# Optimization experiments

Hardware: AMD Instinct MI355X
Metric: run time of the kernel (lower is better)

## Reference

```python
import jax, jax.numpy as jnp
import numpy as np

B, N, U = 4, 4096, 512


def setup_inputs() -> dict:
    key = jax.random.key(0)
    ks = jax.random.split(key, 5)
    s = 1.0 / np.sqrt(U)
    return {
        "x": jax.random.normal(ks[0], (B, N, U), dtype=jnp.float32),
        "Wq": jax.random.normal(ks[1], (U, U), dtype=jnp.float32) * s,
        "bq": jnp.zeros((U,), dtype=jnp.float32),
        "Wk": jax.random.normal(ks[2], (U, U), dtype=jnp.float32) * s,
        "bk": jnp.zeros((U,), dtype=jnp.float32),
        "Wv": jax.random.normal(ks[3], (U, U), dtype=jnp.float32) * s,
        "bv": jnp.zeros((U,), dtype=jnp.float32),
        "Wp": jax.random.normal(ks[4], (U, U), dtype=jnp.float32) * s,
        "bp": jnp.zeros((U,), dtype=jnp.float32),
    }


def reference(x, Wq, bq, Wk, bk, Wv, bv, Wp, bp):
    # x: [B, N, U] single-head self-attention with residual
    scale = jnp.asarray(x.shape[-1], jnp.float32) ** -0.5
    q = x @ Wq + bq
    k = x @ Wk + bk
    v = x @ Wv + bv
    scores = jnp.einsum("bnd,bmd->bnm", q, k) * scale  # [B, N, N]
    attn = jax.nn.softmax(scores, axis=-1)
    ctx = jnp.einsum("bnm,bmd->bnd", attn, v)
    return x + (ctx @ Wp + bp)
```

## Files before the change

kernel.cpp:

```cpp
#include <hip/hip_runtime.h>
#include <hip/hip_bf16.h>
#include <math.h>

#define NB 4
#define NN 4096
#define UU 512

using short8  = __attribute__((ext_vector_type(8))) short;
using bf16x8  = __attribute__((ext_vector_type(8))) __bf16;
using floatx4 = __attribute__((ext_vector_type(4))) float;

__device__ __forceinline__ floatx4 mfma16(short8 a, short8 b, floatx4 c) {
    return __builtin_amdgcn_mfma_f32_16x16x32_bf16(
        __builtin_bit_cast(bf16x8, a), __builtin_bit_cast(bf16x8, b), c, 0, 0, 0);
}

__device__ __forceinline__ unsigned short f2bf(float f) {
    union { float f; unsigned u; } v; v.f = f;
    return (unsigned short)((v.u + 0x7fffu + ((v.u >> 16) & 1u)) >> 16);
}
__device__ __forceinline__ float bf2f(unsigned short s) {
    union { unsigned u; float f; } v; v.u = ((unsigned)s) << 16; return v.f;
}

#define GLL16(gp, lp) __builtin_amdgcn_global_load_lds( \
    (const __attribute__((address_space(1))) void*)(gp), \
    (__attribute__((address_space(3))) void*)(lp), 16, 0, 0)

__global__ void __launch_bounds__(256) k_cvt_x(const float* __restrict__ x,
                                               unsigned short* __restrict__ xb) {
    int i = (blockIdx.x * 256 + threadIdx.x) * 4;
    float4 v = *(const float4*)(x + i);
    ushort4 o;
    o.x = f2bf(v.x); o.y = f2bf(v.y); o.z = f2bf(v.z); o.w = f2bf(v.w);
    *(ushort4*)(xb + i) = o;
}

__global__ void __launch_bounds__(256) k_cvt_w(const float* __restrict__ W,
                                               unsigned short* __restrict__ WT) {
    int idx = blockIdx.x * 256 + threadIdx.x;
    int n = idx >> 9, k = idx & 511;
    WT[idx] = f2bf(W[k * 512 + n]);
}

__global__ void __launch_bounds__(256, 2) k_proj(
    const unsigned short* __restrict__ Xb,
    const unsigned short* __restrict__ WqT, const unsigned short* __restrict__ WkT,
    const unsigned short* __restrict__ WvT,
    const float* __restrict__ bq, const float* __restrict__ bk, const float* __restrict__ bv,
    unsigned short* __restrict__ Q, unsigned short* __restrict__ K8,
    unsigned short* __restrict__ V8)
{
    __shared__ __align__(16) unsigned short As[128 * 32];
    __shared__ __align__(16) unsigned short Bs[128 * 32];
    const int z = blockIdx.z;
    const unsigned short* WT = (z == 0) ? WqT : (z == 1) ? WkT : WvT;
    const float* bias = (z == 0) ? bq : (z == 1) ? bk : bv;
    const int t = threadIdx.x, wave = t >> 6, lane = t & 63;
    const int quad = lane >> 4, l16 = lane & 15;
    const int m0 = blockIdx.x * 128, n0 = blockIdx.y * 128;
    const int wm = wave >> 1, wn = wave & 1;

    const int srow = wave * 32 + (lane >> 2);
    const int scol = (lane & 3) * 8;
    const unsigned short* gA = Xb + (size_t)(m0 + srow) * UU + scol;
    const unsigned short* gB = WT + (size_t)(n0 + srow) * UU + scol;
    unsigned short* lA = As + wave * 1024;
    unsigned short* lB = Bs + wave * 1024;

    floatx4 acc[4][4] = {};

    for (int k0 = 0; k0 < UU; k0 += 32) {
        GLL16(gA + k0, lA);
        GLL16(gA + k0 + 16 * UU, lA + 512);
        GLL16(gB + k0, lB);
        GLL16(gB + k0 + 16 * UU, lB + 512);
        __syncthreads();
        short8 a[4], b[4];
        #pragma unroll
        for (int i = 0; i < 4; i++)
            a[i] = *(const short8*)(As + (wm * 64 + i * 16 + l16) * 32 + quad * 8);
        #pragma unroll
        for (int j = 0; j < 4; j++)
            b[j] = *(const short8*)(Bs + (wn * 64 + j * 16 + l16) * 32 + quad * 8);
        #pragma unroll
        for (int i = 0; i < 4; i++)
            #pragma unroll
            for (int j = 0; j < 4; j++)
                acc[i][j] = mfma16(a[i], b[j], acc[i][j]);
        __syncthreads();
    }

    #pragma unroll
    for (int j = 0; j < 4; j++) {
        const int n = n0 + wn * 64 + j * 16 + l16;
        const float bv_ = bias[n];
        #pragma unroll
        for (int i = 0; i < 4; i++) {
            const int mb = m0 + wm * 64 + i * 16 + quad * 4;
            const int bb = mb >> 12, tok = mb & (NN - 1);
            if (z == 0) {
                #pragma unroll
                for (int r = 0; r < 4; r++)
                    Q[(size_t)(mb + r) * UU + n] = f2bf(acc[i][j][r] + bv_);
            } else if (z == 1) {
                const size_t base = (size_t)bb * NN * UU + (size_t)(n >> 3) * (NN * 8)
                                  + (size_t)tok * 8 + (n & 7);
                #pragma unroll
                for (int r = 0; r < 4; r++)
                    K8[base + (size_t)r * 8] = f2bf(acc[i][j][r] + bv_);
            } else {
                ushort4 o;
                o.x = f2bf(acc[i][j][0] + bv_);
                o.y = f2bf(acc[i][j][1] + bv_);
                o.z = f2bf(acc[i][j][2] + bv_);
                o.w = f2bf(acc[i][j][3] + bv_);
                *(ushort4*)(V8 + (size_t)bb * NN * UU + (size_t)(tok >> 3) * (UU * 8)
                            + (size_t)n * 8 + (tok & 7)) = o;
            }
        }
    }
}

__global__ void __launch_bounds__(512, 1) k_flash(
    const unsigned short* __restrict__ Q,
    const unsigned short* __restrict__ K8,
    const unsigned short* __restrict__ V8,
    unsigned short* __restrict__ ctx)
{
    __shared__ __align__(16) unsigned short Ks[64 * 64 * 8];
    __shared__ __align__(16) unsigned short Vs[8 * 512 * 8];
    __shared__ __align__(16) float S_lds[64 * 68];
    __shared__ __align__(16) unsigned short P_lds[64 * 72];
    __shared__ float m_lds[64], l_lds[64], a_lds[64];

    const int b = blockIdx.y;
    const int q0 = blockIdx.x * 64;
    const int t = threadIdx.x;
    const int wave = t >> 6, lane = t & 63, quad = lane >> 4, l16 = lane & 15;
    const int qt = wave >> 1;
    const int kh = wave & 1;
    const int dh = wave & 1;

    if (t < 64) { m_lds[t] = -INFINITY; l_lds[t] = 0.f; }

    const unsigned short* qp = Q + (size_t)(b * NN + q0 + qt * 16 + l16) * UU + quad * 8;
    short8 qf[16];
    #pragma unroll
    for (int kk = 0; kk < 16; kk++) qf[kk] = *(const short8*)(qp + kk * 32);

    const unsigned short* K8b = K8 + (size_t)b * NN * UU;
    const unsigned short* V8b = V8 + (size_t)b * NN * UU;

    #pragma unroll
    for (int j = 0; j < 8; j++) {
        const int dc = wave * 8 + j;
        GLL16(K8b + (size_t)dc * (NN * 8) + lane * 8, Ks + dc * 512 + lane * 8);
    }

    floatx4 o[16] = {};
    const float sscale = 0.04419417382415922f * 1.4426950408889634f;

    __syncthreads();

    for (int kt = 0; kt < NN; kt += 64) {
        #pragma unroll
        for (int j = 0; j < 8; j++) {
            const int c = wave * 8 + j;
            GLL16(V8b + (size_t)kt * 512 + (size_t)c * 512 + lane * 8, Vs + c * 512 + lane * 8);
        }

        floatx4 s0 = {}, s1 = {};
        #pragma unroll
        for (int kk = 0; kk < 16; kk++) {
            const unsigned short* kb = Ks + (kk * 4 + quad) * 512 + (kh * 32 + l16) * 8;
            short8 b0 = *(const short8*)(kb);
            short8 b1 = *(const short8*)(kb + 128);
            s0 = mfma16(qf[kk], b0, s0);
            s1 = mfma16(qf[kk], b1, s1);
        }
        #pragma unroll
        for (int i = 0; i < 4; i++) {
            S_lds[(qt * 16 + quad * 4 + i) * 68 + kh * 32 + l16]      = s0[i] * sscale;
            S_lds[(qt * 16 + quad * 4 + i) * 68 + kh * 32 + 16 + l16] = s1[i] * sscale;
        }
        __syncthreads();

        {
            const int row = t >> 3, c8 = (t & 7) * 8;
            const float4* sp = (const float4*)(S_lds + row * 68 + c8);
            float4 va = sp[0], vb = sp[1];
            float mx = fmaxf(fmaxf(fmaxf(va.x, va.y), fmaxf(va.z, va.w)),
                             fmaxf(fmaxf(vb.x, vb.y), fmaxf(vb.z, vb.w)));
            mx = fmaxf(mx, __shfl_xor(mx, 1, 8));
            mx = fmaxf(mx, __shfl_xor(mx, 2, 8));
            mx = fmaxf(mx, __shfl_xor(mx, 4, 8));
            const float m_old = m_lds[row];
            const float m_new = fmaxf(m_old, mx);
            float p[8] = { exp2f(va.x - m_new), exp2f(va.y - m_new),
                           exp2f(va.z - m_new), exp2f(va.w - m_new),
                           exp2f(vb.x - m_new), exp2f(vb.y - m_new),
                           exp2f(vb.z - m_new), exp2f(vb.w - m_new) };
            short8 pv; float sum = 0.f;
            #pragma unroll
            for (int j = 0; j < 8; j++) {
                unsigned short us = f2bf(p[j]);
                pv[j] = (short)us;
                sum += bf2f(us);
            }
            *(short8*)(P_lds + row * 72 + c8) = pv;
            sum += __shfl_xor(sum, 1, 8);
            sum += __shfl_xor(sum, 2, 8);
            sum += __shfl_xor(sum, 4, 8);
            if ((t & 7) == 0) {
                const float alpha = exp2f(m_old - m_new);
                a_lds[row] = alpha;
                m_lds[row] = m_new;
                l_lds[row] = l_lds[row] * alpha + sum;
            }
        }
        __syncthreads();

        if (kt + 64 < NN) {
            #pragma unroll
            for (int j = 0; j < 8; j++) {
                const int dc = wave * 8 + j;
                GLL16(K8b + (size_t)dc * (NN * 8) + (size_t)(kt + 64 + lane) * 8,
                      Ks + dc * 512 + lane * 8);
            }
        }

        float al[4];
        #pragma unroll
        for (int i = 0; i < 4; i++) al[i] = a_lds[qt * 16 + quad * 4 + i];
        #pragma unroll
        for (int dt = 0; dt < 16; dt++)
            #pragma unroll
            for (int i = 0; i < 4; i++) o[dt][i] *= al[i];
        const short8 a0 = *(const short8*)(P_lds + (qt * 16 + l16) * 72 + quad * 8);
        const short8 a1 = *(const short8*)(P_lds + (qt * 16 + l16) * 72 + 32 + quad * 8);
        #pragma unroll
        for (int dt = 0; dt < 16; dt++) {
            const int d = dh * 256 + dt * 16 + l16;
            short8 b0 = *(const short8*)(Vs + quad * 4096 + d * 8);
            short8 b1 = *(const short8*)(Vs + (4 + quad) * 4096 + d * 8);
            o[dt] = mfma16(a0, b0, o[dt]);
            o[dt] = mfma16(a1, b1, o[dt]);
        }
        __syncthreads();
    }

    float linv[4];
    #pragma unroll
    for (int i = 0; i < 4; i++) linv[i] = 1.f / l_lds[qt * 16 + quad * 4 + i];
    #pragma unroll
    for (int dt = 0; dt < 16; dt++) {
        const int d = dh * 256 + dt * 16 + l16;
        #pragma unroll
        for (int i = 0; i < 4; i++)
            ctx[(size_t)(b * NN + q0 + qt * 16 + quad * 4 + i) * UU + d] = f2bf(o[dt][i] * linv[i]);
    }
}

__global__ void __launch_bounds__(256, 2) k_out(
    const unsigned short* __restrict__ Cx,
    const unsigned short* __restrict__ WpT,
    const float* __restrict__ bp,
    const float* __restrict__ x,
    float* __restrict__ out)
{
    __shared__ __align__(16) unsigned short As[128 * 32];
    __shared__ __align__(16) unsigned short Bs[128 * 32];
    const int t = threadIdx.x, wave = t >> 6, lane = t & 63;
    const int quad = lane >> 4, l16 = lane & 15;
    const int m0 = blockIdx.x * 128, n0 = blockIdx.y * 128;
    const int wm = wave >> 1, wn = wave & 1;
    const int srow = wave * 32 + (lane >> 2);
    const int scol = (lane & 3) * 8;
    const unsigned short* gA = Cx + (size_t)(m0 + srow) * UU + scol;
    const unsigned short* gB = WpT + (size_t)(n0 + srow) * UU + scol;
    unsigned short* lA = As + wave * 1024;
    unsigned short* lB = Bs + wave * 1024;

    floatx4 acc[4][4] = {};

    for (int k0 = 0; k0 < UU; k0 += 32) {
        GLL16(gA + k0, lA);
        GLL16(gA + k0 + 16 * UU, lA + 512);
        GLL16(gB + k0, lB);
        GLL16(gB + k0 + 16 * UU, lB + 512);
        __syncthreads();
        short8 a[4], b[4];
        #pragma unroll
        for (int i = 0; i < 4; i++)
            a[i] = *(const short8*)(As + (wm * 64 + i * 16 + l16) * 32 + quad * 8);
        #pragma unroll
        for (int j = 0; j < 4; j++)
            b[j] = *(const short8*)(Bs + (wn * 64 + j * 16 + l16) * 32 + quad * 8);
        #pragma unroll
        for (int i = 0; i < 4; i++)
            #pragma unroll
            for (int j = 0; j < 4; j++)
                acc[i][j] = mfma16(a[i], b[j], acc[i][j]);
        __syncthreads();
    }

    #pragma unroll
    for (int j = 0; j < 4; j++) {
        const int n = n0 + wn * 64 + j * 16 + l16;
        const float bv_ = bp[n];
        #pragma unroll
        for (int i = 0; i < 4; i++) {
            const int mb = m0 + wm * 64 + i * 16 + quad * 4;
            #pragma unroll
            for (int r = 0; r < 4; r++) {
                const size_t idx = (size_t)(mb + r) * UU + n;
                out[idx] = acc[i][j][r] + bv_ + x[idx];
            }
        }
    }
}

extern "C" void kernel_launch(void* const* d_in, const int* in_sizes, int n_in,
                              void* d_out, int out_size, void* d_ws, size_t ws_size,
                              hipStream_t stream)
{
    const float* x  = (const float*)d_in[0];
    const float* Wq = (const float*)d_in[1];
    const float* bq = (const float*)d_in[2];
    const float* Wk = (const float*)d_in[3];
    const float* bk = (const float*)d_in[4];
    const float* Wv = (const float*)d_in[5];
    const float* bv = (const float*)d_in[6];
    const float* Wp = (const float*)d_in[7];
    const float* bp = (const float*)d_in[8];
    float* out = (float*)d_out;

    char* ws = (char*)d_ws;
    unsigned short* Xb  = (unsigned short*)(ws);
    unsigned short* WqT = (unsigned short*)(ws + 16777216);
    unsigned short* WkT = (unsigned short*)(ws + 17301504);
    unsigned short* WvT = (unsigned short*)(ws + 17825792);
    unsigned short* WpT = (unsigned short*)(ws + 18350080);
    unsigned short* Qm  = (unsigned short*)(ws + 18874368);
    unsigned short* K8m = (unsigned short*)(ws + 35651584);
    unsigned short* V8m = (unsigned short*)(ws + 52428800);
    unsigned short* Cx  = (unsigned short*)(ws + 69206016);

    hipLaunchKernelGGL(k_cvt_x, dim3(8192), dim3(256), 0, stream, x, Xb);
    hipLaunchKernelGGL(k_cvt_w, dim3(1024), dim3(256), 0, stream, Wq, WqT);
    hipLaunchKernelGGL(k_cvt_w, dim3(1024), dim3(256), 0, stream, Wk, WkT);
    hipLaunchKernelGGL(k_cvt_w, dim3(1024), dim3(256), 0, stream, Wv, WvT);
    hipLaunchKernelGGL(k_cvt_w, dim3(1024), dim3(256), 0, stream, Wp, WpT);
    hipLaunchKernelGGL(k_proj, dim3(128, 4, 3), dim3(256), 0, stream,
                       Xb, WqT, WkT, WvT, bq, bk, bv, Qm, K8m, V8m);
    hipLaunchKernelGGL(k_flash, dim3(64, 4), dim3(512), 0, stream, Qm, K8m, V8m, Cx);
    hipLaunchKernelGGL(k_out, dim3(128, 4), dim3(256), 0, stream, Cx, WpT, bp, x, out);
}
```

Before: 374.6 us.

## Restructure flash kernel waves to split head dim and keys, merge weight conversions

Each wave in the attention kernel now computes two 16-row query tiles over half the head dimension, with QK partial scores combined through LDS atomic adds. Each wave also handles one key half for the PV product, and the two key-half partials are summed through LDS at the end. This is meant to reuse each K and V fragment across two query tiles and so cut LDS reads per MFMA. The cost is atomic adds to shared memory, an extra zeroing pass over the score buffer, and a larger shared-memory footprint (~155KB), which makes the raised launch bound of 2 blocks per CU unlikely to be met. The four weight-conversion launches are also fused into a single launch.

```diff
diff --git a/kernel.cpp b/kernel.cpp
--- a/kernel.cpp
+++ b/kernel.cpp
@@ -36,11 +36,15 @@
     *(ushort4*)(xb + i) = o;
 }
 
-__global__ void __launch_bounds__(256) k_cvt_w(const float* __restrict__ W,
-                                               unsigned short* __restrict__ WT) {
+__global__ void __launch_bounds__(256) k_cvt_w4(
+    const float* __restrict__ Wq, const float* __restrict__ Wk,
+    const float* __restrict__ Wv, const float* __restrict__ Wp,
+    unsigned short* __restrict__ WTbase) {
+    const int z = blockIdx.y;
+    const float* W = (z == 0) ? Wq : (z == 1) ? Wk : (z == 2) ? Wv : Wp;
     int idx = blockIdx.x * 256 + threadIdx.x;
     int n = idx >> 9, k = idx & 511;
-    WT[idx] = f2bf(W[k * 512 + n]);
+    WTbase[(size_t)z * 262144 + idx] = f2bf(W[k * 512 + n]);
 }
 
 __global__ void __launch_bounds__(256, 2) k_proj(
@@ -122,32 +126,42 @@
     }
 }
 
-__global__ void __launch_bounds__(512, 1) k_flash(
+__global__ void __launch_bounds__(512, 2) k_flash(
     const unsigned short* __restrict__ Q,
     const unsigned short* __restrict__ K8,
     const unsigned short* __restrict__ V8,
     unsigned short* __restrict__ ctx)
 {
-    __shared__ __align__(16) unsigned short Ks[64 * 64 * 8];
-    __shared__ __align__(16) unsigned short Vs[8 * 512 * 8];
-    __shared__ __align__(16) float S_lds[64 * 68];
-    __shared__ __align__(16) unsigned short P_lds[64 * 72];
-    __shared__ float m_lds[64], l_lds[64], a_lds[64];
+    __shared__ __align__(16) char smem[158464];
+    unsigned short* Ks = (unsigned short*)smem;
+    unsigned short* Vs = (unsigned short*)(smem + 65536);
+    float*          S_f = (float*)(smem + 131072);
+    unsigned short* P_l = (unsigned short*)(smem + 148480);
+    float*          m_l = (float*)(smem + 157696);
+    float*          l_l = m_l + 64;
+    float*          a_l = m_l + 128;
 
     const int b = blockIdx.y;
     const int q0 = blockIdx.x * 64;
     const int t = threadIdx.x;
     const int wave = t >> 6, lane = t & 63, quad = lane >> 4, l16 = lane & 15;
-    const int qt = wave >> 1;
+    const int qg = wave >> 2;
+    const int half = (wave >> 1) & 1;
     const int kh = wave & 1;
-    const int dh = wave & 1;
-
-    if (t < 64) { m_lds[t] = -INFINITY; l_lds[t] = 0.f; }
-
-    const unsigned short* qp = Q + (size_t)(b * NN + q0 + qt * 16 + l16) * UU + quad * 8;
+
+    if (t < 64) { m_l[t] = -INFINITY; l_l[t] = 0.f; }
+    { const int row = t >> 3, c = (t & 7) * 8;
+      *(float4*)(S_f + row * 68 + c) = float4{0,0,0,0};
+      *(float4*)(S_f + row * 68 + c + 4) = float4{0,0,0,0}; }
+
+    const unsigned short* qp = Q + (size_t)(b * NN + q0 + qg * 32 + l16) * UU
+                             + half * 256 + quad * 8;
     short8 qf[16];
     #pragma unroll
-    for (int kk = 0; kk < 16; kk++) qf[kk] = *(const short8*)(qp + kk * 32);
+    for (int qt = 0; qt < 2; qt++)
+        #pragma unroll
+        for (int kk = 0; kk < 8; kk++)
+            qf[qt * 8 + kk] = *(const short8*)(qp + qt * 16 * UU + kk * 32);
 
     const unsigned short* K8b = K8 + (size_t)b * NN * UU;
     const unsigned short* V8b = V8 + (size_t)b * NN * UU;
@@ -158,7 +172,7 @@
         GLL16(K8b + (size_t)dc * (NN * 8) + lane * 8, Ks + dc * 512 + lane * 8);
     }
 
-    floatx4 o[16] = {};
+    floatx4 o[2][16] = {};
     const float sscale = 0.04419417382415922f * 1.4426950408889634f;
 
     __syncthreads();
@@ -170,32 +184,40 @@
             GLL16(V8b + (size_t)kt * 512 + (size_t)c * 512 + lane * 8, Vs + c * 512 + lane * 8);
         }
 
-        floatx4 s0 = {}, s1 = {};
-        #pragma unroll
-        for (int kk = 0; kk < 16; kk++) {
-            const unsigned short* kb = Ks + (kk * 4 + quad) * 512 + (kh * 32 + l16) * 8;
-            short8 b0 = *(const short8*)(kb);
-            short8 b1 = *(const short8*)(kb + 128);
-            s0 = mfma16(qf[kk], b0, s0);
-            s1 = mfma16(qf[kk], b1, s1);
-        }
-        #pragma unroll
-        for (int i = 0; i < 4; i++) {
-            S_lds[(qt * 16 + quad * 4 + i) * 68 + kh * 32 + l16]      = s0[i] * sscale;
-            S_lds[(qt * 16 + quad * 4 + i) * 68 + kh * 32 + 16 + l16] = s1[i] * sscale;
-        }
+        floatx4 sacc[2][2] = {};
+        #pragma unroll
+        for (int kk = 0; kk < 8; kk++) {
+            #pragma unroll
+            for (int k2 = 0; k2 < 2; k2++) {
+                const int dc = half * 32 + kk * 4 + quad;
+                const int key = kh * 32 + k2 * 16 + l16;
+                short8 bfrag = *(const short8*)(Ks + dc * 512 + key * 8);
+                sacc[0][k2] = mfma16(qf[kk],     bfrag, sacc[0][k2]);
+                sacc[1][k2] = mfma16(qf[8 + kk], bfrag, sacc[1][k2]);
+            }
+        }
+        #pragma unroll
+        for (int qt = 0; qt < 2; qt++)
+            #pragma unroll
+            for (int k2 = 0; k2 < 2; k2++) {
+                const int row = qg * 32 + qt * 16 + quad * 4;
+                const int col = kh * 32 + k2 * 16 + l16;
+                #pragma unroll
+                for (int i = 0; i < 4; i++)
+                    atomicAdd(&S_f[(row + i) * 68 + col], sacc[qt][k2][i] * sscale);
+            }
         __syncthreads();
 
         {
             const int row = t >> 3, c8 = (t & 7) * 8;
-            const float4* sp = (const float4*)(S_lds + row * 68 + c8);
+            const float4* sp = (const float4*)(S_f + row * 68 + c8);
             float4 va = sp[0], vb = sp[1];
             float mx = fmaxf(fmaxf(fmaxf(va.x, va.y), fmaxf(va.z, va.w)),
                              fmaxf(fmaxf(vb.x, vb.y), fmaxf(vb.z, vb.w)));
             mx = fmaxf(mx, __shfl_xor(mx, 1, 8));
             mx = fmaxf(mx, __shfl_xor(mx, 2, 8));
             mx = fmaxf(mx, __shfl_xor(mx, 4, 8));
-            const float m_old = m_lds[row];
+            const float m_old = m_l[row];
             const float m_new = fmaxf(m_old, mx);
             float p[8] = { exp2f(va.x - m_new), exp2f(va.y - m_new),
                            exp2f(va.z - m_new), exp2f(va.w - m_new),
@@ -208,18 +230,22 @@
                 pv[j] = (short)us;
                 sum += bf2f(us);
             }
-            *(short8*)(P_lds + row * 72 + c8) = pv;
+            *(short8*)(P_l + row * 72 + c8) = pv;
             sum += __shfl_xor(sum, 1, 8);
             sum += __shfl_xor(sum, 2, 8);
             sum += __shfl_xor(sum, 4, 8);
             if ((t & 7) == 0) {
                 const float alpha = exp2f(m_old - m_new);
-                a_lds[row] = alpha;
-                m_lds[row] = m_new;
-                l_lds[row] = l_lds[row] * alpha + sum;
-            }
-        }
-        __syncthreads();
+                a_l[row] = alpha;
+                m_l[row] = m_new;
+                l_l[row] = l_l[row] * alpha + sum;
+            }
+        }
+        __syncthreads();
+
+        { const int row = t >> 3, c = (t & 7) * 8;
+          *(float4*)(S_f + row * 68 + c) = float4{0,0,0,0};
+          *(float4*)(S_f + row * 68 + c + 4) = float4{0,0,0,0}; }
 
         if (kt + 64 < NN) {
             #pragma unroll
@@ -230,35 +256,66 @@
             }
         }
 
-        float al[4];
-        #pragma unroll
-        for (int i = 0; i < 4; i++) al[i] = a_lds[qt * 16 + quad * 4 + i];
-        #pragma unroll
-        for (int dt = 0; dt < 16; dt++)
-            #pragma unroll
-            for (int i = 0; i < 4; i++) o[dt][i] *= al[i];
-        const short8 a0 = *(const short8*)(P_lds + (qt * 16 + l16) * 72 + quad * 8);
-        const short8 a1 = *(const short8*)(P_lds + (qt * 16 + l16) * 72 + 32 + quad * 8);
+        float al[8];
+        #pragma unroll
+        for (int qt = 0; qt < 2; qt++)
+            #pragma unroll
+            for (int i = 0; i < 4; i++)
+                al[qt * 4 + i] = a_l[qg * 32 + qt * 16 + quad * 4 + i];
+        #pragma unroll
+        for (int qt = 0; qt < 2; qt++)
+            #pragma unroll
+            for (int dt = 0; dt < 16; dt++)
+                #pragma unroll
+                for (int i = 0; i < 4; i++)
+                    o[qt][dt][i] *= al[qt * 4 + i];
+
+        short8 pa[2];
+        #pragma unroll
+        for (int qt = 0; qt < 2; qt++)
+            pa[qt] = *(const short8*)(P_l + (qg * 32 + qt * 16 + l16) * 72 + kh * 32 + quad * 8);
         #pragma unroll
         for (int dt = 0; dt < 16; dt++) {
-            const int d = dh * 256 + dt * 16 + l16;
-            short8 b0 = *(const short8*)(Vs + quad * 4096 + d * 8);
-            short8 b1 = *(const short8*)(Vs + (4 + quad) * 4096 + d * 8);
-            o[dt] = mfma16(a0, b0, o[dt]);
-            o[dt] = mfma16(a1, b1, o[dt]);
-        }
-        __syncthreads();
-    }
-
-    float linv[4];
-    #pragma unroll
-    for (int i = 0; i < 4; i++) linv[i] = 1.f / l_lds[qt * 16 + quad * 4 + i];
-    #pragma unroll
-    for (int dt = 0; dt < 16; dt++) {
-        const int d = dh * 256 + dt * 16 + l16;
-        #pragma unroll
-        for (int i = 0; i < 4; i++)
-            ctx[(size_t)(b * NN + q0 + qt * 16 + quad * 4 + i) * UU + d] = f2bf(o[dt][i] * linv[i]);
+            const int d = half * 256 + dt * 16 + l16;
+            short8 vb = *(const short8*)(Vs + (kh * 4 + quad) * 4096 + d * 8);
+            o[0][dt] = mfma16(pa[0], vb, o[0][dt]);
+            o[1][dt] = mfma16(pa[1], vb, o[1][dt]);
+        }
+        __syncthreads();
+    }
+
+    float* Obuf = (float*)smem;
+    if (kh == 0) {
+        #pragma unroll
+        for (int qt = 0; qt < 2; qt++)
+            #pragma unroll
+            for (int dt = 0; dt < 16; dt++) {
+                const int d = half * 256 + dt * 16 + l16;
+                #pragma unroll
+                for (int i = 0; i < 4; i++)
+                    Obuf[(qg * 32 + qt * 16 + quad * 4 + i) * 512 + d] = o[qt][dt][i];
+            }
+    }
+    __syncthreads();
+    if (kh == 1) {
+        float linv[8];
+        #pragma unroll
+        for (int qt = 0; qt < 2; qt++)
+            #pragma unroll
+            for (int i = 0; i < 4; i++)
+                linv[qt * 4 + i] = 1.f / l_l[qg * 32 + qt * 16 + quad * 4 + i];
+        #pragma unroll
+        for (int qt = 0; qt < 2; qt++)
+            #pragma unroll
+            for (int dt = 0; dt < 16; dt++) {
+                const int d = half * 256 + dt * 16 + l16;
+                #pragma unroll
+                for (int i = 0; i < 4; i++) {
+                    const int row = qg * 32 + qt * 16 + quad * 4 + i;
+                    const float val = (o[qt][dt][i] + Obuf[row * 512 + d]) * linv[qt * 4 + i];
+                    ctx[(size_t)(b * NN + q0 + row) * UU + d] = f2bf(val);
+                }
+            }
     }
 }
 
@@ -338,20 +395,18 @@
 
     char* ws = (char*)d_ws;
     unsigned short* Xb  = (unsigned short*)(ws);
-    unsigned short* WqT = (unsigned short*)(ws + 16777216);
-    unsigned short* WkT = (unsigned short*)(ws + 17301504);
-    unsigned short* WvT = (unsigned short*)(ws + 17825792);
-    unsigned short* WpT = (unsigned short*)(ws + 18350080);
+    unsigned short* WTb = (unsigned short*)(ws + 16777216);
+    unsigned short* WqT = WTb;
+    unsigned short* WkT = WTb + 262144;
+    unsigned short* WvT = WTb + 524288;
+    unsigned short* WpT = WTb + 786432;
     unsigned short* Qm  = (unsigned short*)(ws + 18874368);
     unsigned short* K8m = (unsigned short*)(ws + 35651584);
     unsigned short* V8m = (unsigned short*)(ws + 52428800);
     unsigned short* Cx  = (unsigned short*)(ws + 69206016);
 
     hipLaunchKernelGGL(k_cvt_x, dim3(8192), dim3(256), 0, stream, x, Xb);
-    hipLaunchKernelGGL(k_cvt_w, dim3(1024), dim3(256), 0, stream, Wq, WqT);
-    hipLaunchKernelGGL(k_cvt_w, dim3(1024), dim3(256), 0, stream, Wk, WkT);
-    hipLaunchKernelGGL(k_cvt_w, dim3(1024), dim3(256), 0, stream, Wv, WvT);
-    hipLaunchKernelGGL(k_cvt_w, dim3(1024), dim3(256), 0, stream, Wp, WpT);
+    hipLaunchKernelGGL(k_cvt_w4, dim3(1024, 4), dim3(256), 0, stream, Wq, Wk, Wv, Wp, WTb);
     hipLaunchKernelGGL(k_proj, dim3(128, 4, 3), dim3(256), 0, stream,
                        Xb, WqT, WkT, WvT, bq, bk, bv, Qm, K8m, V8m);
     hipLaunchKernelGGL(k_flash, dim3(64, 4), dim3(512), 0, stream, Qm, K8m, V8m, Cx);
```

Measured after the change: 1.028 ms. +174.4%, slower.
